# Kernel optimization log

Measured on AMD Instinct MI355X. Metric: run time of the kernel, lower is better.

## Reference

```python
import jax, jax.numpy as jnp
import numpy as np

B, T_MAX, U_MAX, V = 8, 256, 128, 512
NULL_INDEX = 0


def setup_inputs() -> dict:
    key = jax.random.key(0)
    k1, k2, k3, k4 = jax.random.split(key, 4)
    logits = jax.random.normal(k1, (B, T_MAX, U_MAX + 1, V), dtype=jnp.float32)
    y = jax.random.randint(k2, (B, U_MAX), 1, V, dtype=jnp.int32)  # non-blank labels
    T_len = jax.random.randint(k3, (B,), T_MAX // 2, T_MAX + 1, dtype=jnp.int32)
    U_len = jax.random.randint(k4, (B,), U_MAX // 2, U_MAX + 1, dtype=jnp.int32)
    return {"logits": logits, "y": y, "T_len": T_len, "U_len": U_len}


def _rnnt_loss(logits, y, T_len, T_len_unused=None, U_len=None):
    raise NotImplementedError


def reference(logits, y, T_len, U_len):
    # logits: (B, T, U+1, V) raw joiner output; apply log_softmax as in compute_loss
    logp = jax.nn.log_softmax(logits, axis=-1)
    Bn = logits.shape[0]
    blank = logp[..., NULL_INDEX]                                   # (B, T, U+1)
    # emit[b, t, u] = logp[b, t, u, y[b, u]] for u in [0, U_max)
    emit = jnp.take_along_axis(
        logp[:, :, :-1, :], y[:, None, :, None], axis=3)[..., 0]    # (B, T, U)
    # ce[b, t, u] = sum_{k<u} emit[b, t, k] (cumulative emission log-prob)
    ce_all = jnp.concatenate(
        [jnp.zeros((Bn, logits.shape[1], 1), logp.dtype),
         jnp.cumsum(emit, axis=2)], axis=2)                          # (B, T, U+1)

    # Row t=0: alpha[0, u] = sum_{k<u} emit[0, k]
    row0 = ce_all[:, 0, :]                                           # (B, U+1)

    # Row recursion (vectorized over u via log-domain prefix trick):
    # alpha[t, u] = logsumexp_{u'<=u}( a[u'] + ce[t, u] - ce[t, u'] ),
    # with a[u'] = alpha[t-1, u'] + blank[t-1, u'].
    def step(row_prev, xs):
        blank_prev, ce_t = xs                # each (B, U+1)
        a = row_prev + blank_prev
        row = ce_t + jax.lax.associative_scan(jnp.logaddexp, a - ce_t, axis=1)
        return row, row

    xs = (jnp.moveaxis(blank[:, :-1, :], 0, 1),   # (T-1, B, U+1)
          jnp.moveaxis(ce_all[:, 1:, :], 0, 1))   # (T-1, B, U+1)
    _, rows = jax.lax.scan(step, row0, xs)
    alpha = jnp.moveaxis(jnp.concatenate([row0[None], rows], axis=0), 0, 1)  # (B, T, U+1)

    bidx = jnp.arange(Bn)
    log_probs = alpha[bidx, T_len - 1, U_len] + blank[bidx, T_len - 1, U_len]
    return -jnp.mean(log_probs)
```

## Files before the change

### kernel.cpp

```cpp
#include <hip/hip_runtime.h>

#define BN   8
#define TMAX 256
#define UMAX 128
#define U1   129
#define VV   512
#define SD   392
#define PS   132
#define NEG  -1e30f
#define PF   4

__device__ __forceinline__ float logaddexpf_(float a, float b) {
    float mx = fmaxf(a, b);
    float d  = fabsf(a - b);
    return mx + __logf(1.0f + __expf(-d));
}

__global__ __launch_bounds__(256) void lse_extract(
        const float* __restrict__ logits,
        const int*   __restrict__ y,
        const int*   __restrict__ Tl,
        const int*   __restrict__ Ul,
        float* __restrict__ blankD,
        float* __restrict__ emitD) {
    int lane = threadIdx.x & 63;
    int row  = blockIdx.x * 4 + (threadIdx.x >> 6);
    if (row >= BN * TMAX * U1) return;
    int b   = row / (TMAX * U1);
    int rem = row - b * (TMAX * U1);
    int t   = rem / U1;
    int u   = rem - t * U1;
    if (t >= Tl[b] || u > Ul[b]) return;

    const float4* base = (const float4*)(logits + (size_t)row * VV);
    float4 r0 = base[lane * 2];
    float4 r1 = base[lane * 2 + 1];

    float m = fmaxf(fmaxf(fmaxf(r0.x, r0.y), fmaxf(r0.z, r0.w)),
                    fmaxf(fmaxf(r1.x, r1.y), fmaxf(r1.z, r1.w)));
#pragma unroll
    for (int off = 32; off > 0; off >>= 1) m = fmaxf(m, __shfl_xor(m, off));

    float s = __expf(r0.x - m) + __expf(r0.y - m) + __expf(r0.z - m) + __expf(r0.w - m)
            + __expf(r1.x - m) + __expf(r1.y - m) + __expf(r1.z - m) + __expf(r1.w - m);
#pragma unroll
    for (int off = 32; off > 0; off >>= 1) s += __shfl_xor(s, off);

    float lse = m + __logf(s);
    int sd = t + u;
    if (lane == 0)
        blankD[((size_t)b * SD + sd) * PS + u] = r0.x - lse;
    if (u < UMAX) {
        int yv = y[b * UMAX + u];
        if ((yv >> 3) == lane) {
            int e = yv & 7;
            float v = (e == 0) ? r0.x : (e == 1) ? r0.y : (e == 2) ? r0.z : (e == 3) ? r0.w
                    : (e == 4) ? r1.x : (e == 5) ? r1.y : (e == 6) ? r1.z : r1.w;
            emitD[((size_t)b * SD + sd) * PS + (u + 1)] = v - lse;
        }
    }
}

__global__ __launch_bounds__(512) void dp_fused(
        const float* __restrict__ blankD,
        const float* __restrict__ emitD,
        const int*   __restrict__ Tlp,
        const int*   __restrict__ Ulp,
        float* __restrict__ out) {
    __shared__ float part[BN];
    int w = threadIdx.x >> 6;
    int L = threadIdx.x & 63;
    int Tl = Tlp[w], Ul = Ulp[w];
    int dend = Tl - 1 + Ul;
    const float* bD = blankD + (size_t)w * SD * PS;
    const float* eD = emitD  + (size_t)w * SD * PS;

    int  u0 = 2 * L, u1 = 2 * L + 1;
    bool lx = (L == 63);

    float p0 = (L == 0) ? 0.0f : NEG;
    float p1 = NEG, px = NEG;

    float rb0[PF], rb1[PF], re0[PF], re1[PF], rbx[PF], rex[PF];
#pragma unroll
    for (int i = 0; i < PF; ++i) {
        float2 fb = *(const float2*)(bD + i * PS + u0);
        float2 fe = *(const float2*)(eD + i * PS + u0);
        rb0[i] = fb.x; rb1[i] = fb.y; re0[i] = fe.x; re1[i] = fe.y;
        rbx[i] = lx ? bD[i * PS + 128] : NEG;
        rex[i] = lx ? eD[i * PS + 128] : NEG;
    }

    for (int d = 1; d <= dend; ++d) {
        int r = (d - 1) & (PF - 1);
        float b0 = rb0[r], b1 = rb1[r], e0 = re0[r], e1 = re1[r];
        float bx = rbx[r], ex = rex[r];

        float pm1 = __shfl_up(p1, 1);
        if (L == 0) pm1 = NEG;

        int ulo = d - (Tl - 1); if (ulo < 0) ulo = 0;
        int uhi = (d < Ul) ? d : Ul;

        float c0 = logaddexpf_(p0 + b0, pm1 + e0);
        float c1 = logaddexpf_(p1 + b1, p0  + e1);
        float cx = logaddexpf_(px + bx, p1  + ex);

        p0 = (u0 >= ulo && u0 <= uhi) ? c0 : NEG;
        p1 = (u1 >= ulo && u1 <= uhi) ? c1 : NEG;
        px = (lx && 128 >= ulo && 128 <= uhi) ? cx : NEG;

        int s = d - 1 + PF;
        float2 fb = *(const float2*)(bD + s * PS + u0);
        float2 fe = *(const float2*)(eD + s * PS + u0);
        rb0[r] = fb.x; rb1[r] = fb.y; re0[r] = fe.x; re1[r] = fe.y;
        if (lx) { rbx[r] = bD[s * PS + 128]; rex[r] = eD[s * PS + 128]; }
    }

    bool own;
    float afin;
    if (Ul == 128) { own = lx; afin = px; }
    else           { own = (L == (Ul >> 1)); afin = (Ul & 1) ? p1 : p0; }
    if (own) {
        float lp = afin + bD[(size_t)dend * PS + Ul];
        part[w] = lp;
    }
    __syncthreads();
    if (threadIdx.x == 0) {
        float acc = 0.0f;
#pragma unroll
        for (int i = 0; i < BN; ++i) acc += part[i];
        *out = -acc * (1.0f / BN);
    }
}

extern "C" void kernel_launch(void* const* d_in, const int* in_sizes, int n_in,
                              void* d_out, int out_size, void* d_ws, size_t ws_size,
                              hipStream_t stream) {
    const float* logits = (const float*)d_in[0];
    const int*   y      = (const int*)d_in[1];
    const int*   Tl     = (const int*)d_in[2];
    const int*   Ul     = (const int*)d_in[3];
    float* out = (float*)d_out;

    float* blankD = (float*)d_ws;
    float* emitD  = blankD + (size_t)BN * SD * PS;

    int rows = BN * TMAX * U1;
    lse_extract<<<dim3((rows + 3) / 4), dim3(256), 0, stream>>>(
        logits, y, Tl, Ul, blankD, emitD);
    dp_fused<<<dim3(1), dim3(BN * 64), 0, stream>>>(blankD, emitD, Tl, Ul, out);
}
```

Measured before the change: 891.3 us.

## Interleave blank/emit into float4 per lane and deepen DP prefetch ring

The intermediate layout is changed so each lane's blank and emit pairs sit together in one float4, with the u=128 column stored separately as a float2. The DP kernel then issues one vector load per lane per diagonal instead of several scalar and float2 loads. The prefetch depth is doubled to 8 and the loop is fully unrolled over a fixed trip count of 384 with a capture at dend, so ring indices become static registers. The cost is running every wave for the maximum number of diagonals regardless of its actual length, and reading up to PF entries past the stored diagonals.

```diff
diff --git a/kernel.cpp b/kernel.cpp
--- a/kernel.cpp
+++ b/kernel.cpp
@@ -6,9 +6,9 @@
 #define U1   129
 #define VV   512
 #define SD   392
-#define PS   132
+#define DMAX 384
 #define NEG  -1e30f
-#define PF   4
+#define PF   8
 
 __device__ __forceinline__ float logaddexpf_(float a, float b) {
     float mx = fmaxf(a, b);
@@ -21,8 +21,8 @@
         const int*   __restrict__ y,
         const int*   __restrict__ Tl,
         const int*   __restrict__ Ul,
-        float* __restrict__ blankD,
-        float* __restrict__ emitD) {
+        float* __restrict__ cF,
+        float* __restrict__ xF) {
     int lane = threadIdx.x & 63;
     int row  = blockIdx.x * 4 + (threadIdx.x >> 6);
     if (row >= BN * TMAX * U1) return;
@@ -47,23 +47,28 @@
     for (int off = 32; off > 0; off >>= 1) s += __shfl_xor(s, off);
 
     float lse = m + __logf(s);
-    int sd = t + u;
-    if (lane == 0)
-        blankD[((size_t)b * SD + sd) * PS + u] = r0.x - lse;
+    size_t cb = (size_t)b * SD + (t + u);
+    if (lane == 0) {
+        float bl = r0.x - lse;
+        if (u < 128) cF[(cb * 64 + (u >> 1)) * 4 + (u & 1)] = bl;
+        else         xF[cb * 2 + 0] = bl;
+    }
     if (u < UMAX) {
         int yv = y[b * UMAX + u];
         if ((yv >> 3) == lane) {
             int e = yv & 7;
             float v = (e == 0) ? r0.x : (e == 1) ? r0.y : (e == 2) ? r0.z : (e == 3) ? r0.w
                     : (e == 4) ? r1.x : (e == 5) ? r1.y : (e == 6) ? r1.z : r1.w;
-            emitD[((size_t)b * SD + sd) * PS + (u + 1)] = v - lse;
+            int uc = u + 1;
+            if (uc < 128) cF[(cb * 64 + (uc >> 1)) * 4 + 2 + (uc & 1)] = v - lse;
+            else          xF[cb * 2 + 1] = v - lse;
         }
     }
 }
 
 __global__ __launch_bounds__(512) void dp_fused(
-        const float* __restrict__ blankD,
-        const float* __restrict__ emitD,
+        const float4* __restrict__ cD,
+        const float2* __restrict__ xD,
         const int*   __restrict__ Tlp,
         const int*   __restrict__ Ulp,
         float* __restrict__ out) {
@@ -72,58 +77,54 @@
     int L = threadIdx.x & 63;
     int Tl = Tlp[w], Ul = Ulp[w];
     int dend = Tl - 1 + Ul;
-    const float* bD = blankD + (size_t)w * SD * PS;
-    const float* eD = emitD  + (size_t)w * SD * PS;
-
+    const float4* c4 = cD + (size_t)w * SD * 64;
+    const float2* x2 = xD + (size_t)w * SD;
+    bool lx = (L == 63);
     int  u0 = 2 * L, u1 = 2 * L + 1;
-    bool lx = (L == 63);
+    int  Tm1 = Tl - 1;
 
     float p0 = (L == 0) ? 0.0f : NEG;
     float p1 = NEG, px = NEG;
+    float a0 = NEG, a1 = NEG, ax = NEG;
 
-    float rb0[PF], rb1[PF], re0[PF], re1[PF], rbx[PF], rex[PF];
+    float4 ring[PF];
+    float2 xr[PF];
 #pragma unroll
     for (int i = 0; i < PF; ++i) {
-        float2 fb = *(const float2*)(bD + i * PS + u0);
-        float2 fe = *(const float2*)(eD + i * PS + u0);
-        rb0[i] = fb.x; rb1[i] = fb.y; re0[i] = fe.x; re1[i] = fe.y;
-        rbx[i] = lx ? bD[i * PS + 128] : NEG;
-        rex[i] = lx ? eD[i * PS + 128] : NEG;
+        ring[i] = c4[i * 64 + L];
+        xr[i]   = lx ? x2[i] : make_float2(NEG, NEG);
     }
 
-    for (int d = 1; d <= dend; ++d) {
-        int r = (d - 1) & (PF - 1);
-        float b0 = rb0[r], b1 = rb1[r], e0 = re0[r], e1 = re1[r];
-        float bx = rbx[r], ex = rex[r];
-
-        float pm1 = __shfl_up(p1, 1);
-        if (L == 0) pm1 = NEG;
-
-        int ulo = d - (Tl - 1); if (ulo < 0) ulo = 0;
-        int uhi = (d < Ul) ? d : Ul;
-
-        float c0 = logaddexpf_(p0 + b0, pm1 + e0);
-        float c1 = logaddexpf_(p1 + b1, p0  + e1);
-        float cx = logaddexpf_(px + bx, p1  + ex);
-
-        p0 = (u0 >= ulo && u0 <= uhi) ? c0 : NEG;
-        p1 = (u1 >= ulo && u1 <= uhi) ? c1 : NEG;
-        px = (lx && 128 >= ulo && 128 <= uhi) ? cx : NEG;
-
-        int s = d - 1 + PF;
-        float2 fb = *(const float2*)(bD + s * PS + u0);
-        float2 fe = *(const float2*)(eD + s * PS + u0);
-        rb0[r] = fb.x; rb1[r] = fb.y; re0[r] = fe.x; re1[r] = fe.y;
-        if (lx) { rbx[r] = bD[s * PS + 128]; rex[r] = eD[s * PS + 128]; }
+    for (int dc = 1; dc <= DMAX; dc += PF) {
+#pragma unroll
+        for (int j = 0; j < PF; ++j) {
+            int d = dc + j;
+            float4 f = ring[j];
+            float2 g = xr[j];
+            float pm1 = __shfl_up(p1, 1);
+            if (L == 0) pm1 = NEG;
+            float c0 = logaddexpf_(p0 + f.x, pm1 + f.z);
+            float c1 = logaddexpf_(p1 + f.y, p0  + f.w);
+            float cx = logaddexpf_(px + g.x, p1  + g.y);
+            int ulo = d - Tm1; if (ulo < 0) ulo = 0;
+            int uhi = (d < Ul) ? d : Ul;
+            p0 = (u0 >= ulo && u0 <= uhi) ? c0 : NEG;
+            p1 = (u1 >= ulo && u1 <= uhi) ? c1 : NEG;
+            px = (lx && 128 >= ulo && 128 <= uhi) ? cx : NEG;
+            if (d == dend) { a0 = p0; a1 = p1; ax = px; }
+            int s = d + PF - 1;
+            ring[j] = c4[s * 64 + L];
+            xr[j]   = lx ? x2[s] : make_float2(NEG, NEG);
+        }
     }
 
-    bool own;
-    float afin;
-    if (Ul == 128) { own = lx; afin = px; }
-    else           { own = (L == (Ul >> 1)); afin = (Ul & 1) ? p1 : p0; }
-    if (own) {
-        float lp = afin + bD[(size_t)dend * PS + Ul];
-        part[w] = lp;
+    if (Ul == 128) {
+        if (lx) part[w] = ax + x2[dend].x;
+    } else if (L == (Ul >> 1)) {
+        float af = (Ul & 1) ? a1 : a0;
+        const float* cFv = (const float*)c4;
+        float bl = cFv[((size_t)dend * 64 + (Ul >> 1)) * 4 + (Ul & 1)];
+        part[w] = af + bl;
     }
     __syncthreads();
     if (threadIdx.x == 0) {
@@ -143,11 +144,12 @@
     const int*   Ul     = (const int*)d_in[3];
     float* out = (float*)d_out;
 
-    float* blankD = (float*)d_ws;
-    float* emitD  = blankD + (size_t)BN * SD * PS;
+    float* cF = (float*)d_ws;
+    float* xF = cF + (size_t)BN * SD * 64 * 4;
 
     int rows = BN * TMAX * U1;
     lse_extract<<<dim3((rows + 3) / 4), dim3(256), 0, stream>>>(
-        logits, y, Tl, Ul, blankD, emitD);
-    dp_fused<<<dim3(1), dim3(BN * 64), 0, stream>>>(blankD, emitD, Tl, Ul, out);
+        logits, y, Tl, Ul, cF, xF);
+    dp_fused<<<dim3(1), dim3(BN * 64), 0, stream>>>(
+        (const float4*)cF, (const float2*)xF, Tl, Ul, out);
 }
```

New measurement: 753.0 us. 15.5% less time.
